# Performance work log

Hardware: AMD Instinct MI355X
Metric: run time of the kernel (lower is better)

The kernel has to match this reference:

```python
import jax, jax.numpy as jnp
import numpy as np

SIZE = 8192
NB = 64            # nr_blocks
BS = SIZE // NB    # block_size = 128
NTOK = 4096


def setup_inputs() -> dict:
    key = jax.random.key(0)
    k1, k2, k3, k4 = jax.random.split(key, 4)
    # kaiming_normal on [nb, bs, bs]: fan_in per torch default for 3D is bs*bs? torch
    # kaiming_normal_ uses fan_in = bs (last dim sizes); we just use std=sqrt(2/BS).
    std = np.sqrt(2.0 / BS).astype(np.float32)
    x = jax.random.normal(k1, (NTOK, SIZE), dtype=jnp.float32)
    w1 = jax.random.normal(k2, (NB, BS, BS), dtype=jnp.float32) * std
    w2 = jax.random.normal(k3, (NB, BS, BS), dtype=jnp.float32) * std
    bias = jax.random.uniform(k4, (SIZE,), dtype=jnp.float32, minval=-1.0, maxval=1.0) * np.sqrt(1.0 / SIZE).astype(np.float32)
    return {"x": x, "w1": w1, "w2": w2, "bias": bias}


def _monarch(x, w1, w2, bias):
    B = x.reshape(-1, SIZE).shape[0]
    z = x.reshape(B, NB, BS)
    # first block-diagonal matmul: per-block [B,BS] @ [BS,BS]
    h = jnp.einsum('bkc,kcd->bkd', z, w1)            # [B, NB, BS]
    # Permute(size, NB): (B, NB, BS) -> (B, BS, NB) flattened
    h = h.transpose(0, 2, 1).reshape(B, NB, BS)      # regroup into NB blocks of BS
    # second block-diagonal matmul
    h = jnp.einsum('bkc,kcd->bkd', h, w2)            # [B, NB, BS]
    # Permute(size, BS): reshape (B, BS, NB) -> transpose -> (B, NB, BS)
    h = h.reshape(B, BS, NB).transpose(0, 2, 1)
    return h.reshape(x.shape) + bias


def reference(x, w1, w2, bias):
    return _monarch(x, w1, w2, bias)
```

## Files before the change

kernel.cpp:

```cpp
#include <hip/hip_runtime.h>

#define SZ 8192
#define WT_BYTES ((size_t)128 * 16384 * 2)

typedef short short8 __attribute__((ext_vector_type(8)));
typedef float f32x4 __attribute__((ext_vector_type(4)));

static __device__ __forceinline__ unsigned short f2bf(float f){
    unsigned u = __float_as_uint(f);
    u += 0x7fffu + ((u >> 16) & 1u);
    return (unsigned short)(u >> 16);
}

__global__ __launch_bounds__(256) void Monarch_prep(const float* __restrict__ w1,
                                                    const float* __restrict__ w2,
                                                    unsigned short* __restrict__ wt)
{
    __shared__ unsigned short T[128][132];
    int blk = blockIdx.x;
    const float* src = (blk < 64) ? (w1 + (size_t)blk * 16384)
                                  : (w2 + (size_t)(blk - 64) * 16384);
    unsigned short* dst = wt + (size_t)blk * 16384;
    int i  = threadIdx.x;
    int cs = i >> 5;
    int p0 = (i & 31) * 4;
    for (int rr = 0; rr < 16; ++rr){
        int c = rr * 8 + cs;
        f32x4 v = *(const f32x4*)(src + c * 128 + p0);
        T[p0 + 0][c] = f2bf(v[0]);
        T[p0 + 1][c] = f2bf(v[1]);
        T[p0 + 2][c] = f2bf(v[2]);
        T[p0 + 3][c] = f2bf(v[3]);
    }
    __syncthreads();
    for (int rr = 0; rr < 16; ++rr){
        int d = rr * 8 + cs;
        ushort4 o;
        o.x = T[d][p0 + 0]; o.y = T[d][p0 + 1]; o.z = T[d][p0 + 2]; o.w = T[d][p0 + 3];
        *(ushort4*)(dst + d * 128 + p0) = o;
    }
}

__global__ __launch_bounds__(512, 2) void Monarch_main(const float* __restrict__ x,
                                                       const unsigned short* __restrict__ w1T,
                                                       const unsigned short* __restrict__ w2T,
                                                       const float* __restrict__ bias,
                                                       float* __restrict__ out)
{
    __shared__ __align__(16) unsigned short s[32 * 2048];

    int b     = blockIdx.x;
    int xcd   = b & 7;
    int local = b >> 3;
    int g     = local & 3;
    int tgrp  = (xcd << 4) | (local >> 2);
    int t0    = tgrp << 5;
    int k0    = g << 4;
    int d0    = g << 5;

    int tid = threadIdx.x;
    int w   = tid >> 6;
    int l   = tid & 63;
    int m   = l & 15;
    int q   = l >> 4;

    const float* xrow0 = x + (size_t)(t0 + m) * SZ + q * 8;
    const float* xrow1 = xrow0 + (size_t)16 * SZ;
    for (int jt = 0; jt < 8; ++jt){
        int j = (jt << 3) | w;
        f32x4 acc00 = {0.f,0.f,0.f,0.f}, acc01 = {0.f,0.f,0.f,0.f};
        f32x4 acc10 = {0.f,0.f,0.f,0.f}, acc11 = {0.f,0.f,0.f,0.f};
        const float* xp0 = xrow0 + j * 128;
        const float* xp1 = xrow1 + j * 128;
        const unsigned short* w1p = w1T + ((size_t)(j * 128 + d0 + m)) * 128 + q * 8;
        #pragma unroll
        for (int ko = 0; ko < 4; ++ko){
            short8 b0 = *(const short8*)(w1p + ko * 32);
            short8 b1 = *(const short8*)(w1p + 16 * 128 + ko * 32);
            f32x4 xa0 = *(const f32x4*)(xp0 + ko * 32);
            f32x4 xb0 = *(const f32x4*)(xp0 + ko * 32 + 4);
            f32x4 xa1 = *(const f32x4*)(xp1 + ko * 32);
            f32x4 xb1 = *(const f32x4*)(xp1 + ko * 32 + 4);
            short8 a0, a1;
            a0[0] = (short)f2bf(xa0[0]); a0[1] = (short)f2bf(xa0[1]);
            a0[2] = (short)f2bf(xa0[2]); a0[3] = (short)f2bf(xa0[3]);
            a0[4] = (short)f2bf(xb0[0]); a0[5] = (short)f2bf(xb0[1]);
            a0[6] = (short)f2bf(xb0[2]); a0[7] = (short)f2bf(xb0[3]);
            a1[0] = (short)f2bf(xa1[0]); a1[1] = (short)f2bf(xa1[1]);
            a1[2] = (short)f2bf(xa1[2]); a1[3] = (short)f2bf(xa1[3]);
            a1[4] = (short)f2bf(xb1[0]); a1[5] = (short)f2bf(xb1[1]);
            a1[6] = (short)f2bf(xb1[2]); a1[7] = (short)f2bf(xb1[3]);
            acc00 = __builtin_amdgcn_mfma_f32_16x16x32_bf16(a0, b0, acc00, 0, 0, 0);
            acc01 = __builtin_amdgcn_mfma_f32_16x16x32_bf16(a0, b1, acc01, 0, 0, 0);
            acc10 = __builtin_amdgcn_mfma_f32_16x16x32_bf16(a1, b0, acc10, 0, 0, 0);
            acc11 = __builtin_amdgcn_mfma_f32_16x16x32_bf16(a1, b1, acc11, 0, 0, 0);
        }
        #pragma unroll
        for (int r = 0; r < 4; ++r){
            int t   = q * 4 + r;
            int gc0 = 8 * m + jt;
            int gc1 = 8 * (16 + m) + jt;
            int gcs0 = gc0 ^ ((gc0 >> 3) & 7) ^ (t & 7);
            int gcs1 = gc1 ^ ((gc1 >> 3) & 7) ^ (t & 7);
            s[t * 2048 + gcs0 * 8 + w]        = f2bf(acc00[r]);
            s[t * 2048 + gcs1 * 8 + w]        = f2bf(acc01[r]);
            s[(t + 16) * 2048 + gcs0 * 8 + w] = f2bf(acc10[r]);
            s[(t + 16) * 2048 + gcs1 * 8 + w] = f2bf(acc11[r]);
        }
    }
    __syncthreads();

    f32x4 acc[2][2][8];
    #pragma unroll
    for (int ki = 0; ki < 2; ++ki)
        #pragma unroll
        for (int u = 0; u < 2; ++u)
            #pragma unroll
            for (int nt = 0; nt < 8; ++nt)
                acc[ki][u][nt] = (f32x4){0.f, 0.f, 0.f, 0.f};

    #pragma unroll
    for (int ki = 0; ki < 2; ++ki){
        int kl = w + (ki << 3);
        const unsigned short* w2p = w2T + ((size_t)((k0 + kl) * 128 + m)) * 128 + q * 8;
        #pragma unroll
        for (int ko = 0; ko < 4; ++ko){
            int gc  = kl * 16 + ko * 4 + q;
            int gcs = gc ^ ((gc >> 3) & 7) ^ (m & 7);
            short8 a0 = *(const short8*)(s + m * 2048 + gcs * 8);
            short8 a1 = *(const short8*)(s + (m + 16) * 2048 + gcs * 8);
            #pragma unroll
            for (int nt = 0; nt < 8; ++nt){
                short8 bb = *(const short8*)(w2p + nt * 16 * 128 + ko * 32);
                acc[ki][0][nt] = __builtin_amdgcn_mfma_f32_16x16x32_bf16(a0, bb, acc[ki][0][nt], 0, 0, 0);
                acc[ki][1][nt] = __builtin_amdgcn_mfma_f32_16x16x32_bf16(a1, bb, acc[ki][1][nt], 0, 0, 0);
            }
        }
    }
    __syncthreads();

    float* osb = (float*)s;
    #pragma unroll
    for (int u = 0; u < 2; ++u){
        #pragma unroll
        for (int h = 0; h < 2; ++h){
            if ((q >> 1) == h){
                int tb = (q & 1) * 4;
                #pragma unroll
                for (int ki = 0; ki < 2; ++ki){
                    int kl = w + (ki << 3);
                    #pragma unroll
                    for (int nt = 0; nt < 8; ++nt){
                        int n    = nt * 16 + m;
                        int colc = (n & 63) * 32 + 2 * kl + (n >> 6);
                        int gnum = colc >> 2;
                        #pragma unroll
                        for (int r = 0; r < 4; ++r){
                            int t  = tb + r;
                            int gs = gnum ^ ((gnum >> 3) & 7) ^ (t & 7);
                            osb[t * 2048 + gs * 4 + (colc & 3)] = acc[ki][u][nt][r];
                        }
                    }
                }
            }
            __syncthreads();
            {
                int tr = tid >> 6;
                int cl = tid & 63;
                size_t orow = (size_t)(t0 + u * 16 + 8 * h + tr) * SZ;
                #pragma unroll
                for (int f = 0; f < 8; ++f){
                    int colc = cl * 4 + f * 256;
                    int gnum = colc >> 2;
                    int gs   = gnum ^ ((gnum >> 3) & 7) ^ (tr & 7);
                    f32x4 v  = *(const f32x4*)(osb + tr * 2048 + gs * 4);
                    int gcol = ((colc >> 5) << 7) + (g << 5) + (colc & 31);
                    f32x4 bi = *(const f32x4*)(bias + gcol);
                    *(f32x4*)(out + orow + gcol) = v + bi;
                }
            }
            __syncthreads();
        }
    }
}

__global__ __launch_bounds__(256) void Monarch_fused(const float* __restrict__ x,
                                                     const float* __restrict__ w1,
                                                     const float* __restrict__ w2,
                                                     const float* __restrict__ bias,
                                                     float* __restrict__ out)
{
    __shared__ __align__(16) unsigned short s[16 * 2048];
    __shared__ __align__(16) unsigned short wst[4 * 5120];

    int b    = blockIdx.x;
    int g    = (b & 7) >> 1;
    int tile = ((b >> 3) << 1) | (b & 1);
    int t0   = tile << 4;
    int k0   = g << 4;
    int d0   = g << 5;

    int tid = threadIdx.x;
    int w   = tid >> 6;
    int l   = tid & 63;
    int m   = l & 15;
    int q   = l >> 4;

    unsigned short* wb = wst + w * 5120;
    int srow = l >> 3;
    int dcol = (l & 7) * 4;

    const float* xrow = x + (size_t)(t0 + m) * SZ + q * 8;
    for (int jt = 0; jt < 16; ++jt){
        int j = (jt << 2) | w;
        const float* wsrc = w1 + (size_t)j * 16384 + d0;
        #pragma unroll
        for (int rr = 0; rr < 16; ++rr){
            int c = rr * 8 + srow;
            f32x4 v = *(const f32x4*)(wsrc + c * 128 + dcol);
            #pragma unroll
            for (int i2 = 0; i2 < 4; ++i2)
                wb[(dcol + i2) * 136 + c] = (unsigned short)(__float_as_uint(v[i2]) >> 16);
        }
        f32x4 acc0 = {0.f, 0.f, 0.f, 0.f};
        f32x4 acc1 = {0.f, 0.f, 0.f, 0.f};
        const float* xp = xrow + j * 128;
        #pragma unroll
        for (int ko = 0; ko < 4; ++ko){
            f32x4 xa = *(const f32x4*)(xp + ko * 32);
            f32x4 xb = *(const f32x4*)(xp + ko * 32 + 4);
            short8 a;
            a[0] = (short)f2bf(xa[0]); a[1] = (short)f2bf(xa[1]);
            a[2] = (short)f2bf(xa[2]); a[3] = (short)f2bf(xa[3]);
            a[4] = (short)f2bf(xb[0]); a[5] = (short)f2bf(xb[1]);
            a[6] = (short)f2bf(xb[2]); a[7] = (short)f2bf(xb[3]);
            short8 b0 = *(const short8*)(wb + m * 136 + ko * 32 + q * 8);
            short8 b1 = *(const short8*)(wb + (m + 16) * 136 + ko * 32 + q * 8);
            acc0 = __builtin_amdgcn_mfma_f32_16x16x32_bf16(a, b0, acc0, 0, 0, 0);
            acc1 = __builtin_amdgcn_mfma_f32_16x16x32_bf16(a, b1, acc1, 0, 0, 0);
        }
        #pragma unroll
        for (int nt = 0; nt < 2; ++nt){
            int dl = nt * 16 + m;
            int gc = 8 * dl + (j >> 3);
            #pragma unroll
            for (int r = 0; r < 4; ++r){
                int t   = q * 4 + r;
                int gcs = gc ^ ((gc >> 3) & 7) ^ (t & 7);
                float v = nt ? acc1[r] : acc0[r];
                s[t * 2048 + gcs * 8 + (j & 7)] = f2bf(v);
            }
        }
    }
    __syncthreads();

    f32x4 acc[4][8];
    #pragma unroll
    for (int ki = 0; ki < 4; ++ki)
        #pragma unroll
        for (int nt = 0; nt < 8; ++nt)
            acc[ki][nt] = (f32x4){0.f, 0.f, 0.f, 0.f};

    for (int ki = 0; ki < 4; ++ki){
        int kl = w + (ki << 2);
        const float* w2src = w2 + (size_t)(k0 + kl) * 16384;
        #pragma unroll
        for (int ko = 0; ko < 4; ++ko){
            #pragma unroll
            for (int it = 0; it < 4; ++it){
                int cc = it * 8 + srow;
                const float* rp = w2src + (size_t)(ko * 32 + cc) * 128 + (l & 7) * 16;
                #pragma unroll
                for (int v4 = 0; v4 < 4; ++v4){
                    f32x4 v = *(const f32x4*)(rp + v4 * 4);
                    #pragma unroll
                    for (int i2 = 0; i2 < 4; ++i2)
                        wb[((l & 7) * 16 + v4 * 4 + i2) * 40 + cc] =
                            (unsigned short)(__float_as_uint(v[i2]) >> 16);
                }
            }
            int gc  = kl * 16 + ko * 4 + q;
            int gcs = gc ^ ((gc >> 3) & 7) ^ (m & 7);
            short8 a = *(const short8*)(s + m * 2048 + gcs * 8);
            #pragma unroll
            for (int nt = 0; nt < 8; ++nt){
                short8 bb = *(const short8*)(wb + (nt * 16 + m) * 40 + q * 8);
                acc[ki][nt] = __builtin_amdgcn_mfma_f32_16x16x32_bf16(a, bb, acc[ki][nt], 0, 0, 0);
            }
        }
    }
    __syncthreads();

    float* osb = (float*)s;
    for (int h = 0; h < 2; ++h){
        if ((q >> 1) == h){
            int tb = (q & 1) * 4;
            #pragma unroll
            for (int ki = 0; ki < 4; ++ki){
                int kl = w + (ki << 2);
                #pragma unroll
                for (int nt = 0; nt < 8; ++nt){
                    int n    = nt * 16 + m;
                    int colc = (n & 63) * 32 + 2 * kl + (n >> 6);
                    int gnum = colc >> 2;
                    #pragma unroll
                    for (int r = 0; r < 4; ++r){
                        int t  = tb + r;
                        int gs = gnum ^ ((gnum >> 3) & 7) ^ (t & 7);
                        osb[t * 2048 + gs * 4 + (colc & 3)] = acc[ki][nt][r];
                    }
                }
            }
        }
        __syncthreads();
        {
            int tr = tid >> 5;
            int cl = tid & 31;
            size_t orow = (size_t)(t0 + 8 * h + tr) * SZ;
            #pragma unroll
            for (int f = 0; f < 16; ++f){
                int colc = cl * 4 + f * 128;
                int gnum = colc >> 2;
                int gs   = gnum ^ ((gnum >> 3) & 7) ^ (tr & 7);
                f32x4 v  = *(const f32x4*)(osb + tr * 2048 + gs * 4);
                int gcol = ((colc >> 5) << 7) + (g << 5) + (colc & 31);
                f32x4 bi = *(const f32x4*)(bias + gcol);
                *(f32x4*)(out + orow + gcol) = v + bi;
            }
        }
        __syncthreads();
    }
}

extern "C" void kernel_launch(void* const* d_in, const int* in_sizes, int n_in,
                              void* d_out, int out_size, void* d_ws, size_t ws_size,
                              hipStream_t stream) {
    (void)in_sizes; (void)n_in; (void)out_size;
    const float* x    = (const float*)d_in[0];
    const float* w1   = (const float*)d_in[1];
    const float* w2   = (const float*)d_in[2];
    const float* bias = (const float*)d_in[3];

    if (ws_size >= WT_BYTES) {
        unsigned short* wt = (unsigned short*)d_ws;
        Monarch_prep<<<dim3(128), dim3(256), 0, stream>>>(w1, w2, wt);
        Monarch_main<<<dim3(512), dim3(512), 0, stream>>>(x, wt, wt + (size_t)64 * 16384,
                                                          bias, (float*)d_out);
    } else {
        Monarch_fused<<<dim3(1024), dim3(256), 0, stream>>>(x, w1, w2, bias, (float*)d_out);
    }
}
```

Before: 321.6 us.

## Split fused Monarch kernel into two stages via bf16 global intermediate

Splits the fused main kernel into two kernels. Stage one computes the first block-diagonal matmul and writes the permuted bf16 intermediate (64 MB) to workspace. Stage two stages that intermediate into LDS, using async global_load_lds when the builtin exists, and then runs the second matmul plus the bias epilogue. The aim is to shorten each kernel's live ranges and serialization, at the cost of an extra write and read of the intermediate through HBM and an additional launch. It also requires a much larger workspace, and falls back to the old path when the workspace is too small.

```diff
diff --git a/kernel.cpp b/kernel.cpp
--- a/kernel.cpp
+++ b/kernel.cpp
@@ -2,6 +2,7 @@
 
 #define SZ 8192
 #define WT_BYTES ((size_t)128 * 16384 * 2)
+#define H1_BYTES ((size_t)4096 * 8192 * 2)
 
 typedef short short8 __attribute__((ext_vector_type(8)));
 typedef float f32x4 __attribute__((ext_vector_type(4)));
@@ -41,11 +42,9 @@
     }
 }
 
-__global__ __launch_bounds__(512, 2) void Monarch_main(const float* __restrict__ x,
-                                                       const unsigned short* __restrict__ w1T,
-                                                       const unsigned short* __restrict__ w2T,
-                                                       const float* __restrict__ bias,
-                                                       float* __restrict__ out)
+__global__ __launch_bounds__(512, 2) void Monarch_s1(const float* __restrict__ x,
+                                                     const unsigned short* __restrict__ w1T,
+                                                     unsigned short* __restrict__ h1p)
 {
     __shared__ __align__(16) unsigned short s[32 * 2048];
 
@@ -55,7 +54,6 @@
     int g     = local & 3;
     int tgrp  = (xcd << 4) | (local >> 2);
     int t0    = tgrp << 5;
-    int k0    = g << 4;
     int d0    = g << 5;
 
     int tid = threadIdx.x;
@@ -66,6 +64,7 @@
 
     const float* xrow0 = x + (size_t)(t0 + m) * SZ + q * 8;
     const float* xrow1 = xrow0 + (size_t)16 * SZ;
+    #pragma unroll 2
     for (int jt = 0; jt < 8; ++jt){
         int j = (jt << 3) | w;
         f32x4 acc00 = {0.f,0.f,0.f,0.f}, acc01 = {0.f,0.f,0.f,0.f};
@@ -110,6 +109,71 @@
     }
     __syncthreads();
 
+    unsigned short* hseg = h1p + (size_t)t0 * 8192 + g * 2048;
+    #pragma unroll
+    for (int it = 0; it < 16; ++it){
+        int c = it * 512 + tid;
+        int t = c >> 8;
+        int p = c & 255;
+        *(short8*)(hseg + (size_t)t * 8192 + p * 8) = *(const short8*)(s + c * 8);
+    }
+}
+
+__global__ __launch_bounds__(512, 2) void Monarch_s2(const unsigned short* __restrict__ h1p,
+                                                     const unsigned short* __restrict__ w2T,
+                                                     const float* __restrict__ bias,
+                                                     float* __restrict__ out)
+{
+    __shared__ __align__(16) unsigned short s[32 * 2048];
+
+    int b     = blockIdx.x;
+    int xcd   = b & 7;
+    int local = b >> 3;
+    int g     = local & 3;
+    int tgrp  = (xcd << 4) | (local >> 2);
+    int t0    = tgrp << 5;
+    int k0    = g << 4;
+
+    int tid = threadIdx.x;
+    int w   = tid >> 6;
+    int l   = tid & 63;
+    int m   = l & 15;
+    int q   = l >> 4;
+
+    const unsigned short* hseg = h1p + (size_t)t0 * 8192 + g * 2048;
+
+#if defined(__has_builtin)
+#if __has_builtin(__builtin_amdgcn_global_load_lds)
+#define MONARCH_ASYNC_STAGE 1
+#endif
+#endif
+#ifdef MONARCH_ASYNC_STAGE
+    {
+        int c0w = w * 64;
+        #pragma unroll
+        for (int it = 0; it < 16; ++it){
+            int c0 = it * 512 + c0w;
+            int c  = c0 + l;
+            int t  = c >> 8;
+            int p  = c & 255;
+            const unsigned short* gsrc = hseg + (size_t)t * 8192 + p * 8;
+            __builtin_amdgcn_global_load_lds(
+                (const __attribute__((address_space(1))) void*)gsrc,
+                (__attribute__((address_space(3))) void*)(s + (size_t)c0 * 8),
+                16, 0, 0);
+        }
+    }
+#else
+    #pragma unroll
+    for (int it = 0; it < 16; ++it){
+        int c = it * 512 + tid;
+        int t = c >> 8;
+        int p = c & 255;
+        *(short8*)(s + c * 8) = *(const short8*)(hseg + (size_t)t * 8192 + p * 8);
+    }
+#endif
+    __syncthreads();
+
     f32x4 acc[2][2][8];
     #pragma unroll
     for (int ki = 0; ki < 2; ++ki)
@@ -184,6 +248,149 @@
     }
 }
 
+__global__ __launch_bounds__(512, 2) void Monarch_main(const float* __restrict__ x,
+                                                       const unsigned short* __restrict__ w1T,
+                                                       const unsigned short* __restrict__ w2T,
+                                                       const float* __restrict__ bias,
+                                                       float* __restrict__ out)
+{
+    __shared__ __align__(16) unsigned short s[32 * 2048];
+
+    int b     = blockIdx.x;
+    int xcd   = b & 7;
+    int local = b >> 3;
+    int g     = local & 3;
+    int tgrp  = (xcd << 4) | (local >> 2);
+    int t0    = tgrp << 5;
+    int k0    = g << 4;
+    int d0    = g << 5;
+
+    int tid = threadIdx.x;
+    int w   = tid >> 6;
+    int l   = tid & 63;
+    int m   = l & 15;
+    int q   = l >> 4;
+
+    const float* xrow0 = x + (size_t)(t0 + m) * SZ + q * 8;
+    const float* xrow1 = xrow0 + (size_t)16 * SZ;
+    for (int jt = 0; jt < 8; ++jt){
+        int j = (jt << 3) | w;
+        f32x4 acc00 = {0.f,0.f,0.f,0.f}, acc01 = {0.f,0.f,0.f,0.f};
+        f32x4 acc10 = {0.f,0.f,0.f,0.f}, acc11 = {0.f,0.f,0.f,0.f};
+        const float* xp0 = xrow0 + j * 128;
+        const float* xp1 = xrow1 + j * 128;
+        const unsigned short* w1p = w1T + ((size_t)(j * 128 + d0 + m)) * 128 + q * 8;
+        #pragma unroll
+        for (int ko = 0; ko < 4; ++ko){
+            short8 b0 = *(const short8*)(w1p + ko * 32);
+            short8 b1 = *(const short8*)(w1p + 16 * 128 + ko * 32);
+            f32x4 xa0 = *(const f32x4*)(xp0 + ko * 32);
+            f32x4 xb0 = *(const f32x4*)(xp0 + ko * 32 + 4);
+            f32x4 xa1 = *(const f32x4*)(xp1 + ko * 32);
+            f32x4 xb1 = *(const f32x4*)(xp1 + ko * 32 + 4);
+            short8 a0, a1;
+            a0[0] = (short)f2bf(xa0[0]); a0[1] = (short)f2bf(xa0[1]);
+            a0[2] = (short)f2bf(xa0[2]); a0[3] = (short)f2bf(xa0[3]);
+            a0[4] = (short)f2bf(xb0[0]); a0[5] = (short)f2bf(xb0[1]);
+            a0[6] = (short)f2bf(xb0[2]); a0[7] = (short)f2bf(xb0[3]);
+            a1[0] = (short)f2bf(xa1[0]); a1[1] = (short)f2bf(xa1[1]);
+            a1[2] = (short)f2bf(xa1[2]); a1[3] = (short)f2bf(xa1[3]);
+            a1[4] = (short)f2bf(xb1[0]); a1[5] = (short)f2bf(xb1[1]);
+            a1[6] = (short)f2bf(xb1[2]); a1[7] = (short)f2bf(xb1[3]);
+            acc00 = __builtin_amdgcn_mfma_f32_16x16x32_bf16(a0, b0, acc00, 0, 0, 0);
+            acc01 = __builtin_amdgcn_mfma_f32_16x16x32_bf16(a0, b1, acc01, 0, 0, 0);
+            acc10 = __builtin_amdgcn_mfma_f32_16x16x32_bf16(a1, b0, acc10, 0, 0, 0);
+            acc11 = __builtin_amdgcn_mfma_f32_16x16x32_bf16(a1, b1, acc11, 0, 0, 0);
+        }
+        #pragma unroll
+        for (int r = 0; r < 4; ++r){
+            int t   = q * 4 + r;
+            int gc0 = 8 * m + jt;
+            int gc1 = 8 * (16 + m) + jt;
+            int gcs0 = gc0 ^ ((gc0 >> 3) & 7) ^ (t & 7);
+            int gcs1 = gc1 ^ ((gc1 >> 3) & 7) ^ (t & 7);
+            s[t * 2048 + gcs0 * 8 + w]        = f2bf(acc00[r]);
+            s[t * 2048 + gcs1 * 8 + w]        = f2bf(acc01[r]);
+            s[(t + 16) * 2048 + gcs0 * 8 + w] = f2bf(acc10[r]);
+            s[(t + 16) * 2048 + gcs1 * 8 + w] = f2bf(acc11[r]);
+        }
+    }
+    __syncthreads();
+
+    f32x4 acc[2][2][8];
+    #pragma unroll
+    for (int ki = 0; ki < 2; ++ki)
+        #pragma unroll
+        for (int u = 0; u < 2; ++u)
+            #pragma unroll
+            for (int nt = 0; nt < 8; ++nt)
+                acc[ki][u][nt] = (f32x4){0.f, 0.f, 0.f, 0.f};
+
+    #pragma unroll
+    for (int ki = 0; ki < 2; ++ki){
+        int kl = w + (ki << 3);
+        const unsigned short* w2p = w2T + ((size_t)((k0 + kl) * 128 + m)) * 128 + q * 8;
+        #pragma unroll
+        for (int ko = 0; ko < 4; ++ko){
+            int gc  = kl * 16 + ko * 4 + q;
+            int gcs = gc ^ ((gc >> 3) & 7) ^ (m & 7);
+            short8 a0 = *(const short8*)(s + m * 2048 + gcs * 8);
+            short8 a1 = *(const short8*)(s + (m + 16) * 2048 + gcs * 8);
+            #pragma unroll
+            for (int nt = 0; nt < 8; ++nt){
+                short8 bb = *(const short8*)(w2p + nt * 16 * 128 + ko * 32);
+                acc[ki][0][nt] = __builtin_amdgcn_mfma_f32_16x16x32_bf16(a0, bb, acc[ki][0][nt], 0, 0, 0);
+                acc[ki][1][nt] = __builtin_amdgcn_mfma_f32_16x16x32_bf16(a1, bb, acc[ki][1][nt], 0, 0, 0);
+            }
+        }
+    }
+    __syncthreads();
+
+    float* osb = (float*)s;
+    #pragma unroll
+    for (int u = 0; u < 2; ++u){
+        #pragma unroll
+        for (int h = 0; h < 2; ++h){
+            if ((q >> 1) == h){
+                int tb = (q & 1) * 4;
+                #pragma unroll
+                for (int ki = 0; ki < 2; ++ki){
+                    int kl = w + (ki << 3);
+                    #pragma unroll
+                    for (int nt = 0; nt < 8; ++nt){
+                        int n    = nt * 16 + m;
+                        int colc = (n & 63) * 32 + 2 * kl + (n >> 6);
+                        int gnum = colc >> 2;
+                        #pragma unroll
+                        for (int r = 0; r < 4; ++r){
+                            int t  = tb + r;
+                            int gs = gnum ^ ((gnum >> 3) & 7) ^ (t & 7);
+                            osb[t * 2048 + gs * 4 + (colc & 3)] = acc[ki][u][nt][r];
+                        }
+                    }
+                }
+            }
+            __syncthreads();
+            {
+                int tr = tid >> 6;
+                int cl = tid & 63;
+                size_t orow = (size_t)(t0 + u * 16 + 8 * h + tr) * SZ;
+                #pragma unroll
+                for (int f = 0; f < 8; ++f){
+                    int colc = cl * 4 + f * 256;
+                    int gnum = colc >> 2;
+                    int gs   = gnum ^ ((gnum >> 3) & 7) ^ (tr & 7);
+                    f32x4 v  = *(const f32x4*)(osb + tr * 2048 + gs * 4);
+                    int gcol = ((colc >> 5) << 7) + (g << 5) + (colc & 31);
+                    f32x4 bi = *(const f32x4*)(bias + gcol);
+                    *(f32x4*)(out + orow + gcol) = v + bi;
+                }
+            }
+            __syncthreads();
+        }
+    }
+}
+
 __global__ __launch_bounds__(256) void Monarch_fused(const float* __restrict__ x,
                                                      const float* __restrict__ w1,
                                                      const float* __restrict__ w2,
@@ -341,7 +548,14 @@
     const float* w2   = (const float*)d_in[2];
     const float* bias = (const float*)d_in[3];
 
-    if (ws_size >= WT_BYTES) {
+    if (ws_size >= WT_BYTES + H1_BYTES) {
+        unsigned short* wt  = (unsigned short*)d_ws;
+        unsigned short* h1p = wt + (size_t)128 * 16384;
+        Monarch_prep<<<dim3(128), dim3(256), 0, stream>>>(w1, w2, wt);
+        Monarch_s1<<<dim3(512), dim3(512), 0, stream>>>(x, wt, h1p);
+        Monarch_s2<<<dim3(512), dim3(512), 0, stream>>>(h1p, wt + (size_t)64 * 16384,
+                                                        bias, (float*)d_out);
+    } else if (ws_size >= WT_BYTES) {
         unsigned short* wt = (unsigned short*)d_ws;
         Monarch_prep<<<dim3(128), dim3(256), 0, stream>>>(w1, w2, wt);
         Monarch_main<<<dim3(512), dim3(512), 0, stream>>>(x, wt, wt + (size_t)64 * 16384,
```

After: 355.5 us. +10.6%, slower.
